# Kernel optimization log

Hardware: AMD Instinct MI355X
Metric: run time of the kernel (lower is better)

The kernel has to match this reference:

```python
import jax, jax.numpy as jnp
import numpy as np

EPS = 1e-5
SLOPE = 0.01  # torch LeakyReLU default

def _conv(x, w, b, stride):
    # x: [B,C,L], w: [O,I,3]
    y = jax.lax.conv_general_dilated(x, w, (stride,), [(1, 1)],
                                     dimension_numbers=("NCH", "OIH", "NCH"))
    return y + b[None, :, None]

def _bn(x, g, b, m, v):
    # eval-mode BatchNorm1d with running stats
    inv = jax.lax.rsqrt(v + EPS)
    return (x - m[None, :, None]) * (g * inv)[None, :, None] + b[None, :, None]

def _lrelu(x):
    return jnp.where(x >= 0, x, SLOPE * x)

def setup_inputs() -> dict:
    key = jax.random.key(0)
    ks = jax.random.split(key, 32)
    B, C, L = 32, 256, 2048
    K, D = 4096, 128
    d = {}
    d["x"] = jax.random.normal(ks[0], (B, C, L), dtype=jnp.float32)
    # conv weights [O,I,3]
    d["w1"] = jax.random.normal(ks[1], (256, 256, 3), jnp.float32) * 0.03
    d["b1"] = jax.random.normal(ks[2], (256,), jnp.float32) * 0.01
    d["w2"] = jax.random.normal(ks[3], (512, 256, 3), jnp.float32) * 0.03
    d["b2"] = jax.random.normal(ks[4], (512,), jnp.float32) * 0.01
    d["w3"] = jax.random.normal(ks[5], (512, 512, 3), jnp.float32) * 0.02
    d["b3"] = jax.random.normal(ks[6], (512,), jnp.float32) * 0.01
    d["w4"] = jax.random.normal(ks[7], (D, 512, 3), jnp.float32) * 0.02
    d["b4"] = jax.random.normal(ks[8], (D,), jnp.float32) * 0.01
    for i, ch in enumerate([256, 512, 512, D]):
        d[f"g{i+1}"] = 1.0 + 0.1 * jax.random.normal(ks[9 + 4 * i], (ch,), jnp.float32)
        d[f"be{i+1}"] = 0.1 * jax.random.normal(ks[10 + 4 * i], (ch,), jnp.float32)
        d[f"m{i+1}"] = 0.1 * jax.random.normal(ks[11 + 4 * i], (ch,), jnp.float32)
        d[f"v{i+1}"] = 0.5 + jax.random.uniform(ks[12 + 4 * i], (ch,), jnp.float32)
    d["emb"] = jax.random.uniform(ks[30], (K, D), jnp.float32,
                                  minval=-1.0 / K, maxval=1.0 / K)
    return d

def reference(x, w1, b1, w2, b2, w3, b3, w4, b4,
              g1, be1, m1, v1, g2, be2, m2, v2,
              g3, be3, m3, v3, g4, be4, m4, v4, emb):
    h = _lrelu(_bn(_conv(x, w1, b1, 2), g1, be1, m1, v1))   # [B,256,L/2]
    h = _lrelu(_bn(_conv(h, w2, b2, 2), g2, be2, m2, v2))   # [B,512,L/4]
    h = _lrelu(_bn(_conv(h, w3, b3, 2), g3, be3, m3, v3))   # [B,512,L/8]
    h = _lrelu(_bn(_conv(h, w4, b4, 1), g4, be4, m4, v4))   # [B,D,L/8]
    flat = jnp.transpose(h, (0, 2, 1)).reshape(-1, h.shape[1])  # [N,D]
    # squared-distance expansion: ||f||^2 + ||e||^2 - 2 f.e
    dist = (jnp.sum(flat * flat, axis=1, keepdims=True)
            + jnp.sum(emb * emb, axis=1)
            - 2.0 * flat @ emb.T)                            # [N,K]
    codes = jnp.argmin(dist, axis=1)
    return codes, dist
```

## Files before the change

kernel.cpp:

```cpp
#include <hip/hip_runtime.h>
#include <cstdint>
#include <math.h>

#define EPS_BN 1e-5f
#define SLOPE 0.01f
#define C14 6.103515625e-5f
#define SC14 16384.0f
#define HMIN 6.103515625e-5f

typedef __attribute__((ext_vector_type(8))) _Float16 half8;
typedef __attribute__((ext_vector_type(8))) short short8;
typedef __attribute__((ext_vector_type(16))) float f32x16;
typedef __attribute__((ext_vector_type(4))) float f32x4;

__device__ __forceinline__ void split16(float v, unsigned short& uh,
                                        unsigned short& ul) {
    _Float16 h = (_Float16)v;
    if (fabsf(v) < HMIN) h = (_Float16)0.0f;
    float rem = v - (float)h;
    _Float16 l = (_Float16)(rem * SC14);
    uh = __builtin_bit_cast(unsigned short, h);
    ul = __builtin_bit_cast(unsigned short, l);
}

typedef const __attribute__((address_space(1))) unsigned int* gas_ptr;
typedef __attribute__((address_space(3))) unsigned int* las_ptr;
__device__ __forceinline__ void glds16(const void* g, void* l) {
    __builtin_amdgcn_global_load_lds((gas_ptr)g, (las_ptr)l, 16, 0, 0);
}

template<int N>
__device__ __forceinline__ void vm_wait() {
    if constexpr (N == 0)      asm volatile("s_waitcnt vmcnt(0)" ::: "memory");
    else if constexpr (N == 8) asm volatile("s_waitcnt vmcnt(8)" ::: "memory");
    else if constexpr (N == 9) asm volatile("s_waitcnt vmcnt(9)" ::: "memory");
}
__device__ __forceinline__ void raw_bar() {
    asm volatile("" ::: "memory");
    __builtin_amdgcn_s_barrier();
    asm volatile("" ::: "memory");
}

__global__ __launch_bounds__(256)
void wprep_all(const float* __restrict__ w1, short* __restrict__ o1,
               const float* __restrict__ w2, short* __restrict__ o2,
               const float* __restrict__ w3, short* __restrict__ o3,
               const float* __restrict__ w4, short* __restrict__ o4)
{
    const float* w; short* wbuf; int CIN, COUT;
    switch (blockIdx.y) {
        case 0: w = w1; wbuf = o1; CIN = 256; COUT = 256; break;
        case 1: w = w2; wbuf = o2; CIN = 256; COUT = 512; break;
        case 2: w = w3; wbuf = o3; CIN = 512; COUT = 512; break;
        default: w = w4; wbuf = o4; CIN = 512; COUT = 128; break;
    }
    int KST = CIN / 16, OB = COUT / 128;
    int total = KST * OB * 1536;
    for (int sid = blockIdx.x * 256 + threadIdx.x; sid < total;
         sid += gridDim.x * 256) {
        int slot = sid % 1536;
        int kb = sid / 1536;
        int ob = kb % OB, ks = kb / OB;
        int m = slot & 31, hi = (slot >> 5) & 1, mf = (slot >> 6) & 3;
        int ts = slot >> 8;
        int t = ts >> 1, s = ts & 1;
        int oc = ob * 128 + mf * 32 + m;
        int ib = ks * 16 + hi * 8;
        short8 r;
        #pragma unroll
        for (int j = 0; j < 8; ++j) {
            float v = w[((size_t)oc * CIN + ib + j) * 3 + t];
            unsigned short uh, ul;
            split16(v, uh, ul);
            r[j] = (short)(s == 0 ? uh : ul);
        }
        *(short8*)(wbuf + (size_t)sid * 8) = r;
    }
}

__global__ __launch_bounds__(256)
void bnprep_init(
    const float* __restrict__ g1, const float* __restrict__ be1,
    const float* __restrict__ m1, const float* __restrict__ v1,
    const float* __restrict__ b1, float* __restrict__ sc1, float* __restrict__ off1,
    const float* __restrict__ g2, const float* __restrict__ be2,
    const float* __restrict__ m2, const float* __restrict__ v2,
    const float* __restrict__ b2, float* __restrict__ sc2, float* __restrict__ off2,
    const float* __restrict__ g3, const float* __restrict__ be3,
    const float* __restrict__ m3, const float* __restrict__ v3,
    const float* __restrict__ b3, float* __restrict__ sc3, float* __restrict__ off3,
    const float* __restrict__ g4, const float* __restrict__ be4,
    const float* __restrict__ m4, const float* __restrict__ v4,
    const float* __restrict__ b4, float* __restrict__ sc4, float* __restrict__ off4,
    unsigned long long* __restrict__ mp, float* __restrict__ sf)
{
    int bid = blockIdx.x;
    if (bid >= 38) { sf[(bid - 38) * 256 + threadIdx.x] = 0.0f; return; }
    if (bid >= 6) { mp[(bid - 6) * 256 + threadIdx.x] = ~0ULL; return; }
    const float *g, *be, *m, *v, *bias;
    float *sc, *off;
    int c;
    if (bid == 0) {
        g = g1; be = be1; m = m1; v = v1; bias = b1; sc = sc1; off = off1;
        c = threadIdx.x;
    } else if (bid <= 2) {
        g = g2; be = be2; m = m2; v = v2; bias = b2; sc = sc2; off = off2;
        c = (bid - 1) * 256 + threadIdx.x;
    } else if (bid <= 4) {
        g = g3; be = be3; m = m3; v = v3; bias = b3; sc = sc3; off = off3;
        c = (bid - 3) * 256 + threadIdx.x;
    } else {
        g = g4; be = be4; m = m4; v = v4; bias = b4; sc = sc4; off = off4;
        c = threadIdx.x;
        if (c >= 128) return;
    }
    float s = g[c] / sqrtf(v[c] + EPS_BN);
    sc[c] = s;
    off[c] = (bias[c] - m[c]) * s + be[c];
}

__global__ __launch_bounds__(256)
void xsplit(const float* __restrict__ x, short* __restrict__ xpl)
{
    const size_t PL = (size_t)32 * 32 * 2 * 1025 * 8;
    int l = blockIdx.x * 256 + threadIdx.x;
    int g = blockIdx.y, b = blockIdx.z;
    float v[8];
    #pragma unroll
    for (int j = 0; j < 8; ++j)
        v[j] = x[((size_t)b * 256 + g * 8 + j) * 2048 + l];
    int arr = l & 1;
    int slot = arr ? (l + 1) / 2 : l / 2 + 1;
    size_t base = ((((size_t)b * 32 + g) * 2 + arr) * 1025 + slot) * 8;
    short8 rh, rl;
    #pragma unroll
    for (int j = 0; j < 8; ++j) {
        unsigned short uh, ul;
        split16(v[j], uh, ul);
        rh[j] = (short)uh; rl[j] = (short)ul;
    }
    *(short8*)(xpl + base) = rh;
    *(short8*)(xpl + PL + base) = rl;
    if (l == 0) {
        short8 z;
        #pragma unroll
        for (int j = 0; j < 8; ++j) z[j] = 0;
        for (int sg = 0; sg < 2; ++sg)
            for (int a2 = 0; a2 < 2; ++a2)
                *(short8*)(xpl + sg * PL +
                           ((((size_t)b * 32 + g) * 2 + a2) * 1025) * 8) = z;
    }
}

template<int CIN, int COUT, int LIN, int TILE, int EPI>
__global__ __launch_bounds__(512, 1)
void conv_pair(const short* __restrict__ wbuf, const short* __restrict__ xpl,
               const float* __restrict__ scv, const float* __restrict__ offv,
               short* __restrict__ opl)
{
    constexpr int LOUT = LIN / 2;
    constexpr int KST = CIN / 16;
    constexpr int OBS = COUT / 128;
    constexpr int NG = CIN / 8;
    constexpr int SLOTS = LIN / 2 + 1;
    constexpr size_t PLIN = (size_t)32 * NG * 2 * SLOTS * 8;
    constexpr int NF = TILE / 64;
    constexpr int NGo = COUT / 8;
    constexpr int OSLOTS = (EPI == 0) ? (LOUT / 2 + 1) : (LOUT + 2);
    constexpr size_t PLOUT = (size_t)32 * NGo * ((EPI == 0) ? 2 : 1) * OSLOTS * 8;

    constexpr int XOFF = 49152;
    constexpr int BUF  = XOFF + 8 * 2112;
    constexpr int SCOFF = 2 * BUF;
    constexpr int SCNT = (TILE == 128) ? 9 : 8;
    __shared__ __align__(16) char lds[2 * BUF + 2048];

    const int tid = threadIdx.x;
    const int lane = tid & 63;
    const int wv = tid >> 6;
    const int wo = wv >> 2;
    const int wm = (wv >> 1) & 1, wn = wv & 1;
    const int hi = lane >> 5, n32 = lane & 31;
    const int n0 = blockIdx.x * TILE;
    const int oby = blockIdx.y;
    const int o0 = oby * 256;
    const int b = blockIdx.z;

    if (tid < 256) ((float*)(lds + SCOFF))[tid] = scv[o0 + tid];
    else ((float*)(lds + SCOFF + 1024))[tid - 256] = offv[o0 + tid - 256];

    f32x16 acc0[2][2], acc1[2][2];
    #pragma unroll
    for (int i = 0; i < 2; ++i)
        #pragma unroll
        for (int j = 0; j < 2; ++j)
            #pragma unroll
            for (int e = 0; e < 16; ++e) { acc0[i][j][e] = 0.0f; acc1[i][j][e] = 0.0f; }

    auto stage = [&](char* base, int ks) {
        const short* wsrc = wbuf + ((size_t)ks * OBS + (oby * 2 + wo)) * 1536 * 8;
        #pragma unroll
        for (int it = 0; it < 6; ++it) {
            int slot0 = it * 256 + (wv & 3) * 64;
            glds16(wsrc + (size_t)(slot0 + lane) * 8, base + wo * 24576 + slot0 * 16);
        }
        int g0 = ks * 2;
        int sg = wv >> 2, rhi = (wv >> 1) & 1, arr = wv & 1;
        int start = arr ? n0 : (n0 + 1);
        const short* src = xpl + (size_t)sg * PLIN
            + ((((size_t)b * NG + (g0 + rhi)) * 2 + arr) * SLOTS + start) * 8;
        char* dst = base + XOFF + ((sg * 2 + rhi) * 2 + arr) * 2112;
        if (TILE == 128) {
            glds16(src + (size_t)lane * 8, dst);
            glds16(src + (size_t)(64 + lane) * 8, dst + 64 * 16);
            int c2 = arr ? 65 : 64;
            glds16(src + (size_t)(c2 + lane) * 8, dst + c2 * 16);
        } else {
            glds16(src + (size_t)lane * 8, dst);
            int c1 = arr ? 1 : 0;
            glds16(src + (size_t)(c1 + lane) * 8, dst + c1 * 16);
        }
    };

    stage(lds, 0);

    #pragma unroll 1
    for (int ks = 0; ks < KST; ++ks) {
        char* cbase = lds + (ks & 1) * BUF;
        char* nbase = lds + ((ks & 1) ^ 1) * BUF;
        if (ks + 1 < KST) {
            stage(nbase, ks + 1);
            vm_wait<SCNT>();
        } else {
            vm_wait<0>();
        }
        raw_bar();
        __builtin_amdgcn_s_setprio(1);
        #pragma unroll
        for (int t = 0; t < 3; ++t) {
            half8 af[2][2], bx[2][2];
            #pragma unroll
            for (int s = 0; s < 2; ++s) {
                #pragma unroll
                for (int mf = 0; mf < 2; ++mf)
                    af[s][mf] = *(const half8*)(cbase + wo * 24576 +
                        (((t * 2 + s) * 4 + (wm * 2 + mf)) * 64 + lane) * 16);
                int arr = (t == 1) ? 0 : 1;
                int tof = (t == 2) ? 1 : 0;
                #pragma unroll
                for (int nf = 0; nf < NF; ++nf) {
                    int qb = wn * (TILE / 2) + nf * 32 + tof;
                    bx[s][nf] = *(const half8*)(cbase + XOFF + s * 8448
                                                + arr * 2112 + qb * 16
                                                + hi * 4224 + n32 * 16);
                }
            }
            #pragma unroll
            for (int mf = 0; mf < 2; ++mf)
                #pragma unroll
                for (int nf = 0; nf < NF; ++nf) {
                    acc0[mf][nf] = __builtin_amdgcn_mfma_f32_32x32x16_f16(
                        af[0][mf], bx[0][nf], acc0[mf][nf], 0, 0, 0);
                    acc1[mf][nf] = __builtin_amdgcn_mfma_f32_32x32x16_f16(
                        af[0][mf], bx[1][nf], acc1[mf][nf], 0, 0, 0);
                    acc1[mf][nf] = __builtin_amdgcn_mfma_f32_32x32x16_f16(
                        af[1][mf], bx[0][nf], acc1[mf][nf], 0, 0, 0);
                }
        }
        __builtin_amdgcn_s_setprio(0);
        raw_bar();
    }

    #pragma unroll
    for (int half = 0; half < NF; ++half) {
        __syncthreads();
        #pragma unroll
        for (int mf = 0; mf < 2; ++mf)
            #pragma unroll
            for (int r = 0; r < 16; ++r) {
                int ocl = mf * 32 + (r & 3) + 8 * (r >> 2) + 4 * hi;
                *(float*)(lds + wv * 8704 + n32 * 272 + ocl * 4) =
                    acc0[mf][half][r] + C14 * acc1[mf][half][r];
            }
        __syncthreads();
        #pragma unroll
        for (int it = 0; it < 4; ++it) {
            int sl = tid + it * 512;
            int w = sl >> 8, rem = sl & 255, p = rem >> 3, grp = rem & 7;
            int wo_ = w >> 2, wm_ = (w >> 1) & 1, wn_ = w & 1;
            f32x4 v0 = *(f32x4*)(lds + w * 8704 + p * 272 + grp * 32);
            f32x4 v1 = *(f32x4*)(lds + w * 8704 + p * 272 + grp * 32 + 16);
            int ocb = wo_ * 128 + wm_ * 64 + grp * 8;
            f32x4 s0 = *(f32x4*)(lds + SCOFF + ocb * 4);
            f32x4 s1 = *(f32x4*)(lds + SCOFF + ocb * 4 + 16);
            f32x4 q0 = *(f32x4*)(lds + SCOFF + 1024 + ocb * 4);
            f32x4 q1 = *(f32x4*)(lds + SCOFF + 1024 + ocb * 4 + 16);
            float y[8];
            #pragma unroll
            for (int j = 0; j < 4; ++j) {
                float a = v0[j] * s0[j] + q0[j];
                y[j] = a >= 0.0f ? a : SLOPE * a;
                float c = v1[j] * s1[j] + q1[j];
                y[4 + j] = c >= 0.0f ? c : SLOPE * c;
            }
            int pos_abs = n0 + wn_ * (TILE / 2) + half * 32 + p;
            int oc_abs = o0 + ocb;
            short8 rh, rl;
            #pragma unroll
            for (int j = 0; j < 8; ++j) {
                unsigned short uh, ul;
                split16(y[j], uh, ul);
                rh[j] = (short)uh; rl[j] = (short)ul;
            }
            int gq = oc_abs >> 3;
            size_t base;
            if (EPI == 0) {
                int arr = pos_abs & 1;
                int slot = arr ? (pos_abs + 1) / 2 : pos_abs / 2 + 1;
                base = ((((size_t)b * NGo + gq) * 2 + arr) * OSLOTS + slot) * 8;
            } else {
                base = (((size_t)b * NGo + gq) * OSLOTS + (pos_abs + 1)) * 8;
            }
            *(short8*)(opl + base) = rh;
            *(short8*)(opl + PLOUT + base) = rl;
        }
    }

    if (EPI == 0) {
        if (blockIdx.x == 0 && tid < 128) {
            int sg = tid >> 6, r2 = tid & 63, g16 = r2 >> 1, a2 = r2 & 1;
            int gq = oby * 32 + g16;
            short8 z;
            #pragma unroll
            for (int j = 0; j < 8; ++j) z[j] = 0;
            *(short8*)(opl + (size_t)sg * PLOUT +
                       ((((size_t)b * NGo + gq) * 2 + a2) * OSLOTS) * 8) = z;
        }
    } else {
        if (tid < 64 && (blockIdx.x == 0 || blockIdx.x == gridDim.x - 1)) {
            int sg = tid >> 5, g16 = tid & 31;
            int gq = oby * 32 + g16;
            int slot = (blockIdx.x == 0) ? 0 : (OSLOTS - 1);
            short8 z;
            #pragma unroll
            for (int j = 0; j < 8; ++j) z[j] = 0;
            *(short8*)(opl + (size_t)sg * PLOUT +
                       (((size_t)b * NGo + gq) * OSLOTS + slot) * 8) = z;
        }
    }
}

template<int CIN, int COUT, int LIN>
__global__ __launch_bounds__(256, 2)
void conv_s1(const short* __restrict__ wbuf, const short* __restrict__ xpl,
             const float* __restrict__ scv, const float* __restrict__ offv,
             short* __restrict__ fh, short* __restrict__ fl,
             float* __restrict__ sf)
{
    constexpr int KST = CIN / 16;
    constexpr int NG = CIN / 8;
    constexpr int SLOTS = LIN + 2;
    constexpr size_t PLIN = (size_t)32 * NG * SLOTS * 8;

    constexpr int XOFF = 24576;
    constexpr int BUF  = XOFF + 4 * 2112;
    constexpr int SCOFF = 2 * BUF;
    __shared__ __align__(16) char lds[2 * BUF + 1024];

    const int tid = threadIdx.x;
    const int lane = tid & 63;
    const int wv = tid >> 6;
    const int wm = wv >> 1, wn = wv & 1;
    const int hi = lane >> 5, n32 = lane & 31;
    const int n0 = blockIdx.x * 128;
    const int b = blockIdx.z;

    if (tid < 128) {
        ((float*)(lds + SCOFF))[tid] = scv[tid];
        ((float*)(lds + SCOFF + 512))[tid] = offv[tid];
    }

    f32x16 acc0[2][2], acc1[2][2];
    #pragma unroll
    for (int i = 0; i < 2; ++i)
        #pragma unroll
        for (int j = 0; j < 2; ++j)
            #pragma unroll
            for (int e = 0; e < 16; ++e) { acc0[i][j][e] = 0.0f; acc1[i][j][e] = 0.0f; }

    auto stage = [&](char* base, int ks) {
        const short* wsrc = wbuf + (size_t)ks * 1536 * 8;
        #pragma unroll
        for (int it = 0; it < 6; ++it) {
            int slot0 = it * 256 + wv * 64;
            glds16(wsrc + (size_t)(slot0 + lane) * 8, base + slot0 * 16);
        }
        int g0 = ks * 2;
        int sg = wv >> 1, rhi = wv & 1;
        const short* src = xpl + (size_t)sg * PLIN
            + (((size_t)b * NG + (g0 + rhi)) * SLOTS + n0) * 8;
        char* dst = base + XOFF + (sg * 2 + rhi) * 2112;
        glds16(src + (size_t)lane * 8, dst);
        glds16(src + (size_t)(64 + lane) * 8, dst + 64 * 16);
        glds16(src + (size_t)(66 + lane) * 8, dst + 66 * 16);
    };

    stage(lds, 0);

    #pragma unroll 1
    for (int ks = 0; ks < KST; ++ks) {
        char* cbase = lds + (ks & 1) * BUF;
        char* nbase = lds + ((ks & 1) ^ 1) * BUF;
        if (ks + 1 < KST) {
            stage(nbase, ks + 1);
            vm_wait<9>();
        } else {
            vm_wait<0>();
        }
        raw_bar();
        __builtin_amdgcn_s_setprio(1);
        #pragma unroll
        for (int t = 0; t < 3; ++t) {
            half8 af[2][2], bx[2][2];
            #pragma unroll
            for (int s = 0; s < 2; ++s) {
                #pragma unroll
                for (int mf = 0; mf < 2; ++mf)
                    af[s][mf] = *(const half8*)(cbase +
                        (((t * 2 + s) * 4 + (wm * 2 + mf)) * 64 + lane) * 16);
                #pragma unroll
                for (int nf = 0; nf < 2; ++nf) {
                    int qb = wn * 64 + nf * 32 + t;
                    bx[s][nf] = *(const half8*)(cbase + XOFF + s * 4224
                                                + qb * 16 + hi * 2112 + n32 * 16);
                }
            }
            #pragma unroll
            for (int mf = 0; mf < 2; ++mf)
                #pragma unroll
                for (int nf = 0; nf < 2; ++nf) {
                    acc0[mf][nf] = __builtin_amdgcn_mfma_f32_32x32x16_f16(
                        af[0][mf], bx[0][nf], acc0[mf][nf], 0, 0, 0);
                    acc1[mf][nf] = __builtin_amdgcn_mfma_f32_32x32x16_f16(
                        af[0][mf], bx[1][nf], acc1[mf][nf], 0, 0, 0);
                    acc1[mf][nf] = __builtin_amdgcn_mfma_f32_32x32x16_f16(
                        af[1][mf], bx[0][nf], acc1[mf][nf], 0, 0, 0);
                }
        }
        __builtin_amdgcn_s_setprio(0);
        raw_bar();
    }

    #pragma unroll
    for (int half = 0; half < 2; ++half) {
        __syncthreads();
        #pragma unroll
        for (int mf = 0; mf < 2; ++mf)
            #pragma unroll
            for (int r = 0; r < 16; ++r) {
                int ocl = mf * 32 + (r & 3) + 8 * (r >> 2) + 4 * hi;
                *(float*)(lds + wv * 8704 + n32 * 272 + ocl * 4) =
                    acc0[mf][half][r] + C14 * acc1[mf][half][r];
            }
        __syncthreads();
        #pragma unroll
        for (int it = 0; it < 4; ++it) {
            int sl = tid + it * 256;
            int w = sl >> 8, rem = sl & 255, p = rem >> 3, grp = rem & 7;
            int wm_ = w >> 1, wn_ = w & 1;
            f32x4 v0 = *(f32x4*)(lds + w * 8704 + p * 272 + grp * 32);
            f32x4 v1 = *(f32x4*)(lds + w * 8704 + p * 272 + grp * 32 + 16);
            int oclb = wm_ * 64 + grp * 8;
            f32x4 s0 = *(f32x4*)(lds + SCOFF + oclb * 4);
            f32x4 s1 = *(f32x4*)(lds + SCOFF + oclb * 4 + 16);
            f32x4 q0 = *(f32x4*)(lds + SCOFF + 512 + oclb * 4);
            f32x4 q1 = *(f32x4*)(lds + SCOFF + 512 + oclb * 4 + 16);
            float y[8];
            #pragma unroll
            for (int j = 0; j < 4; ++j) {
                float a = v0[j] * s0[j] + q0[j];
                y[j] = a >= 0.0f ? a : SLOPE * a;
                float c = v1[j] * s1[j] + q1[j];
                y[4 + j] = c >= 0.0f ? c : SLOPE * c;
            }
            int pos_abs = n0 + wn_ * 64 + half * 32 + p;
            int n = b * 256 + pos_abs;
            short8 rh, rl;
            float partial = 0.0f;
            #pragma unroll
            for (int j = 0; j < 8; ++j) {
                partial = fmaf(y[j], y[j], partial);
                unsigned short uh, ul;
                split16(y[j], uh, ul);
                rh[j] = (short)uh; rl[j] = (short)ul;
            }
            int g = wm_ * 8 + grp;
            size_t slot = ((((size_t)(n >> 5) * 8 + (g >> 1)) * 2 + (g & 1)) * 32
                           + (n & 31)) * 8;
            *(short8*)(fh + slot) = rh;
            *(short8*)(fl + slot) = rl;
            atomicAdd(sf + n, partial);
        }
    }
}

__global__ __launch_bounds__(256)
void split_kernel(const float* __restrict__ src, int nrows,
                  short* __restrict__ ph, short* __restrict__ pl,
                  float* __restrict__ sumv)
{
    int t = blockIdx.x * 256 + threadIdx.x;
    int n = t >> 4, g = t & 15;
    if (n >= nrows) return;
    const float* rowp = src + (size_t)n * 128 + g * 8;
    float4 v0 = *(const float4*)rowp;
    float4 v1 = *(const float4*)(rowp + 4);
    float vv[8] = {v0.x, v0.y, v0.z, v0.w, v1.x, v1.y, v1.z, v1.w};
    short8 rh, rl;
    float ss = 0.0f;
    #pragma unroll
    for (int j = 0; j < 8; ++j) {
        float v = vv[j];
        ss = fmaf(v, v, ss);
        unsigned short uh, ul;
        split16(v, uh, ul);
        rh[j] = (short)uh; rl[j] = (short)ul;
    }
    int nb = n >> 5, m = n & 31, ks = g >> 1, hi = g & 1;
    size_t slot = ((((size_t)nb * 8 + ks) * 2 + hi) * 32 + m) * 8;
    *(short8*)(ph + slot) = rh;
    *(short8*)(pl + slot) = rl;
    #pragma unroll
    for (int mk = 8; mk; mk >>= 1) ss += __shfl_xor(ss, mk);
    if (g == 0) sumv[n] = ss;
}

__global__ __launch_bounds__(256, 2)
void distmin_kernel(const short* __restrict__ fh, const short* __restrict__ fl,
                    const short* __restrict__ eh, const short* __restrict__ el,
                    const float* __restrict__ sf, const float* __restrict__ se,
                    float* __restrict__ dist, unsigned long long* __restrict__ mp)
{
    __shared__ unsigned long long cand[128 * 64];
    const int tid = threadIdx.x;
    const int lane = tid & 63;
    const int wv = tid >> 6;
    const int wm = wv >> 1, wn = wv & 1;
    const int hi = lane >> 5, n32 = lane & 31;
    const int kb = blockIdx.x;
    const int nb = blockIdx.y;

    f32x16 acc0[2][2], acc1[2][2];
    #pragma unroll
    for (int i = 0; i < 2; ++i)
        #pragma unroll
        for (int j = 0; j < 2; ++j)
            #pragma unroll
            for (int e = 0; e < 16; ++e) { acc0[i][j][e] = 0.0f; acc1[i][j][e] = 0.0f; }

    const short* fb[2][2];
    const short* eb[2][2];
    {
        const short* fpl[2] = {fh, fl};
        const short* epl[2] = {eh, el};
        #pragma unroll
        for (int s = 0; s < 2; ++s) {
            #pragma unroll
            for (int mf = 0; mf < 2; ++mf)
                fb[s][mf] = fpl[s] + (size_t)nb * 16384
                            + ((size_t)(wm * 2 + mf) * 8 * 64 + lane) * 8;
            #pragma unroll
            for (int nf = 0; nf < 2; ++nf)
                eb[s][nf] = epl[s]
                            + ((size_t)(kb * 4 + wn * 2 + nf) * 8 * 64 + lane) * 8;
        }
    }

    #pragma unroll
    for (int ks = 0; ks < 8; ++ks) {
        half8 af[2][2], bx[2][2];
        #pragma unroll
        for (int s = 0; s < 2; ++s) {
            #pragma unroll
            for (int mf = 0; mf < 2; ++mf)
                af[s][mf] = *(const half8*)(fb[s][mf] + ks * 512);
            #pragma unroll
            for (int nf = 0; nf < 2; ++nf)
                bx[s][nf] = *(const half8*)(eb[s][nf] + ks * 512);
        }
        #pragma unroll
        for (int mf = 0; mf < 2; ++mf)
            #pragma unroll
            for (int nf = 0; nf < 2; ++nf) {
                acc0[mf][nf] = __builtin_amdgcn_mfma_f32_32x32x16_f16(
                    af[0][mf], bx[0][nf], acc0[mf][nf], 0, 0, 0);
                acc1[mf][nf] = __builtin_amdgcn_mfma_f32_32x32x16_f16(
                    af[0][mf], bx[1][nf], acc1[mf][nf], 0, 0, 0);
                acc1[mf][nf] = __builtin_amdgcn_mfma_f32_32x32x16_f16(
                    af[1][mf], bx[0][nf], acc1[mf][nf], 0, 0, 0);
            }
    }

    const int n_blk = nb * 128;
    const int kc0 = kb * 128 + wn * 64 + n32;
    const float se0 = se[kc0];
    const float se1 = se[kc0 + 32];
    #pragma unroll
    for (int mf = 0; mf < 2; ++mf) {
        #pragma unroll
        for (int r = 0; r < 16; ++r) {
            int nloc = wm * 64 + mf * 32 + (r & 3) + 8 * (r >> 2) + 4 * hi;
            int n = n_blk + nloc;
            float sfn = sf[n];
            float d0 = acc0[mf][0][r] + C14 * acc1[mf][0][r];
            float d1 = acc0[mf][1][r] + C14 * acc1[mf][1][r];
            float v0 = (sfn + se0) - 2.0f * d0;
            float v1 = (sfn + se1) - 2.0f * d1;
            __builtin_nontemporal_store(v0, &dist[(size_t)n * 4096 + kc0]);
            __builtin_nontemporal_store(v1, &dist[(size_t)n * 4096 + kc0 + 32]);
            unsigned long long p0 =
                (((unsigned long long)__float_as_uint(v0)) << 32) | (unsigned)kc0;
            unsigned long long p1 =
                (((unsigned long long)__float_as_uint(v1)) << 32) | (unsigned)(kc0 + 32);
            unsigned long long p = p1 < p0 ? p1 : p0;
            cand[nloc * 64 + wn * 32 + n32] = p;
        }
    }
    __syncthreads();
    {
        int row = tid >> 1, h = tid & 1;
        unsigned long long best = ~0ULL;
        #pragma unroll
        for (int i = 0; i < 32; ++i) {
            int c = h * 32 + ((i + row) & 31);
            unsigned long long cv = cand[row * 64 + c];
            best = cv < best ? cv : best;
        }
        unsigned lo = (unsigned)best, hw = (unsigned)(best >> 32);
        unsigned lo2 = __shfl_xor(lo, 1), hw2 = __shfl_xor(hw, 1);
        unsigned long long ob = (((unsigned long long)hw2) << 32) | lo2;
        if (ob < best) best = ob;
        if (h == 0) atomicMin(mp + n_blk + row, best);
    }
}

__global__ __launch_bounds__(256)
void codes_kernel(const unsigned long long* __restrict__ mp,
                  float* __restrict__ codes)
{
    int n = blockIdx.x * 256 + threadIdx.x;
    if (n < 8192) codes[n] = (float)(unsigned)(mp[n] & 0xffffffffULL);
}

extern "C" void kernel_launch(void* const* d_in, const int* in_sizes, int n_in,
                              void* d_out, int out_size, void* d_ws, size_t ws_size,
                              hipStream_t stream)
{
    const float* x   = (const float*)d_in[0];
    const float* w1  = (const float*)d_in[1];
    const float* b1  = (const float*)d_in[2];
    const float* w2  = (const float*)d_in[3];
    const float* b2  = (const float*)d_in[4];
    const float* w3  = (const float*)d_in[5];
    const float* b3  = (const float*)d_in[6];
    const float* w4  = (const float*)d_in[7];
    const float* b4  = (const float*)d_in[8];
    const float* g1  = (const float*)d_in[9];
    const float* be1 = (const float*)d_in[10];
    const float* m1  = (const float*)d_in[11];
    const float* v1  = (const float*)d_in[12];
    const float* g2  = (const float*)d_in[13];
    const float* be2 = (const float*)d_in[14];
    const float* m2  = (const float*)d_in[15];
    const float* v2  = (const float*)d_in[16];
    const float* g3  = (const float*)d_in[17];
    const float* be3 = (const float*)d_in[18];
    const float* m3  = (const float*)d_in[19];
    const float* v3  = (const float*)d_in[20];
    const float* g4  = (const float*)d_in[21];
    const float* be4 = (const float*)d_in[22];
    const float* m4  = (const float*)d_in[23];
    const float* v4  = (const float*)d_in[24];
    const float* emb = (const float*)d_in[25];

    float* outf  = (float*)d_out;
    float* codes = outf;
    float* distm = outf + 8192;

    char* wsb = (char*)d_ws;
    short* wb1 = (short*)(wsb + 0);
    short* wb2 = (short*)(wsb + 786432);
    short* wb3 = (short*)(wsb + 2359296);
    short* wb4 = (short*)(wsb + 5505024);
    float* sc1 = (float*)(wsb + 6291456); float* off1 = sc1 + 256;
    float* sc2 = (float*)(wsb + 6293504); float* off2 = sc2 + 512;
    float* sc3 = (float*)(wsb + 6297600); float* off3 = sc3 + 512;
    float* sc4 = (float*)(wsb + 6301696); float* off4 = sc4 + 128;
    short* h1p = (short*)(wsb + 6302720);
    short* fh  = (short*)(wsb + 39922688);
    short* fl  = (short*)(wsb + 42019840);
    short* eh  = (short*)(wsb + 44116992);
    short* el  = (short*)(wsb + 45165568);
    float* sf  = (float*)(wsb + 46214144);
    float* se  = (float*)(wsb + 46246912);
    unsigned long long* mp = (unsigned long long*)(wsb + 46263296);

    char* db = (char*)distm;
    short* xpl = (short*)db;
    short* h2p = (short*)db;
    short* h3p = (short*)(db + 33685504);

    wprep_all<<<dim3(192, 4), 256, 0, stream>>>(w1, wb1, w2, wb2, w3, wb3, w4, wb4);
    bnprep_init<<<70, 256, 0, stream>>>(
        g1, be1, m1, v1, b1, sc1, off1,
        g2, be2, m2, v2, b2, sc2, off2,
        g3, be3, m3, v3, b3, sc3, off3,
        g4, be4, m4, v4, b4, sc4, off4, mp, sf);
    split_kernel<<<256, 256, 0, stream>>>(emb, 4096, eh, el, se);

    xsplit<<<dim3(8, 32, 32), 256, 0, stream>>>(x, xpl);
    conv_pair<256, 256, 2048, 128, 0>
        <<<dim3(8, 1, 32), 512, 0, stream>>>(wb1, xpl, sc1, off1, h1p);
    conv_pair<256, 512, 1024, 128, 0>
        <<<dim3(4, 2, 32), 512, 0, stream>>>(wb2, h1p, sc2, off2, h2p);
    conv_pair<512, 512, 512, 64, 1>
        <<<dim3(4, 2, 32), 512, 0, stream>>>(wb3, h2p, sc3, off3, h3p);
    conv_s1<512, 128, 256>
        <<<dim3(2, 1, 32), 256, 0, stream>>>(wb4, h3p, sc4, off4, fh, fl, sf);

    distmin_kernel<<<dim3(32, 64), 256, 0, stream>>>(fh, fl, eh, el,
                                                     sf, se, distm, mp);
    codes_kernel<<<32, 256, 0, stream>>>(mp, codes);
}
```

Baseline: 261.4 us.

## Fuse input split into first conv, use register-staged prefetch, halve conv4 tile

The standalone xsplit kernel is removed. The first conv now reads raw fp32 input, splits it into fp16 high/low parts and writes them to LDS itself, which avoids a full write and re-read of the split input in global memory. All conv kernels switch from direct global-to-LDS loads to a register-staged scheme: the next stage is loaded into registers during the MFMA work and written to LDS afterwards, followed by __syncthreads. The final stride-1 conv uses 64-wide tiles, doubling its grid from 64 to 128 blocks. The register staging raises register pressure and drops the async LDS-load path, which could hurt the heavier conv kernels.

```diff
diff --git a/kernel.cpp b/kernel.cpp
--- a/kernel.cpp
+++ b/kernel.cpp
@@ -21,24 +21,6 @@
     _Float16 l = (_Float16)(rem * SC14);
     uh = __builtin_bit_cast(unsigned short, h);
     ul = __builtin_bit_cast(unsigned short, l);
-}
-
-typedef const __attribute__((address_space(1))) unsigned int* gas_ptr;
-typedef __attribute__((address_space(3))) unsigned int* las_ptr;
-__device__ __forceinline__ void glds16(const void* g, void* l) {
-    __builtin_amdgcn_global_load_lds((gas_ptr)g, (las_ptr)l, 16, 0, 0);
-}
-
-template<int N>
-__device__ __forceinline__ void vm_wait() {
-    if constexpr (N == 0)      asm volatile("s_waitcnt vmcnt(0)" ::: "memory");
-    else if constexpr (N == 8) asm volatile("s_waitcnt vmcnt(8)" ::: "memory");
-    else if constexpr (N == 9) asm volatile("s_waitcnt vmcnt(9)" ::: "memory");
-}
-__device__ __forceinline__ void raw_bar() {
-    asm volatile("" ::: "memory");
-    __builtin_amdgcn_s_barrier();
-    asm volatile("" ::: "memory");
 }
 
 __global__ __launch_bounds__(256)
@@ -119,42 +101,10 @@
     off[c] = (bias[c] - m[c]) * s + be[c];
 }
 
-__global__ __launch_bounds__(256)
-void xsplit(const float* __restrict__ x, short* __restrict__ xpl)
-{
-    const size_t PL = (size_t)32 * 32 * 2 * 1025 * 8;
-    int l = blockIdx.x * 256 + threadIdx.x;
-    int g = blockIdx.y, b = blockIdx.z;
-    float v[8];
-    #pragma unroll
-    for (int j = 0; j < 8; ++j)
-        v[j] = x[((size_t)b * 256 + g * 8 + j) * 2048 + l];
-    int arr = l & 1;
-    int slot = arr ? (l + 1) / 2 : l / 2 + 1;
-    size_t base = ((((size_t)b * 32 + g) * 2 + arr) * 1025 + slot) * 8;
-    short8 rh, rl;
-    #pragma unroll
-    for (int j = 0; j < 8; ++j) {
-        unsigned short uh, ul;
-        split16(v[j], uh, ul);
-        rh[j] = (short)uh; rl[j] = (short)ul;
-    }
-    *(short8*)(xpl + base) = rh;
-    *(short8*)(xpl + PL + base) = rl;
-    if (l == 0) {
-        short8 z;
-        #pragma unroll
-        for (int j = 0; j < 8; ++j) z[j] = 0;
-        for (int sg = 0; sg < 2; ++sg)
-            for (int a2 = 0; a2 < 2; ++a2)
-                *(short8*)(xpl + sg * PL +
-                           ((((size_t)b * 32 + g) * 2 + a2) * 1025) * 8) = z;
-    }
-}
-
-template<int CIN, int COUT, int LIN, int TILE, int EPI>
+template<int CIN, int COUT, int LIN, int TILE, int EPI, int SRC>
 __global__ __launch_bounds__(512, 1)
 void conv_pair(const short* __restrict__ wbuf, const short* __restrict__ xpl,
+               const float* __restrict__ xraw,
                const float* __restrict__ scv, const float* __restrict__ offv,
                short* __restrict__ opl)
 {
@@ -172,7 +122,6 @@
     constexpr int XOFF = 49152;
     constexpr int BUF  = XOFF + 8 * 2112;
     constexpr int SCOFF = 2 * BUF;
-    constexpr int SCNT = (TILE == 128) ? 9 : 8;
     __shared__ __align__(16) char lds[2 * BUF + 2048];
 
     const int tid = threadIdx.x;
@@ -197,44 +146,98 @@
             #pragma unroll
             for (int e = 0; e < 16; ++e) { acc0[i][j][e] = 0.0f; acc1[i][j][e] = 0.0f; }
 
-    auto stage = [&](char* base, int ks) {
+    short8 rw[6];
+    short8 rxa, rxb, rxc;
+    float rf[8], rf2[8];
+
+    auto stage_load = [&](int ks) {
         const short* wsrc = wbuf + ((size_t)ks * OBS + (oby * 2 + wo)) * 1536 * 8;
         #pragma unroll
-        for (int it = 0; it < 6; ++it) {
-            int slot0 = it * 256 + (wv & 3) * 64;
-            glds16(wsrc + (size_t)(slot0 + lane) * 8, base + wo * 24576 + slot0 * 16);
-        }
-        int g0 = ks * 2;
-        int sg = wv >> 2, rhi = (wv >> 1) & 1, arr = wv & 1;
-        int start = arr ? n0 : (n0 + 1);
-        const short* src = xpl + (size_t)sg * PLIN
-            + ((((size_t)b * NG + (g0 + rhi)) * 2 + arr) * SLOTS + start) * 8;
-        char* dst = base + XOFF + ((sg * 2 + rhi) * 2 + arr) * 2112;
-        if (TILE == 128) {
-            glds16(src + (size_t)lane * 8, dst);
-            glds16(src + (size_t)(64 + lane) * 8, dst + 64 * 16);
-            int c2 = arr ? 65 : 64;
-            glds16(src + (size_t)(c2 + lane) * 8, dst + c2 * 16);
+        for (int it = 0; it < 6; ++it)
+            rw[it] = *(const short8*)(wsrc +
+                      (size_t)(it * 256 + (wv & 3) * 64 + lane) * 8);
+        if constexpr (SRC == 0) {
+            int sg = wv >> 2, rhi = (wv >> 1) & 1, arr = wv & 1;
+            int start = arr ? n0 : (n0 + 1);
+            const short* src = xpl + (size_t)sg * PLIN
+                + ((((size_t)b * NG + (ks * 2 + rhi)) * 2 + arr) * SLOTS + start) * 8;
+            rxa = *(const short8*)(src + (size_t)lane * 8);
+            if constexpr (TILE == 128) {
+                rxb = *(const short8*)(src + (size_t)(64 + lane) * 8);
+                if (arr && lane == 0)
+                    rxc = *(const short8*)(src + (size_t)128 * 8);
+            } else {
+                if (arr && lane == 0)
+                    rxb = *(const short8*)(src + (size_t)64 * 8);
+            }
         } else {
-            glds16(src + (size_t)lane * 8, dst);
-            int c1 = arr ? 1 : 0;
-            glds16(src + (size_t)(c1 + lane) * 8, dst + c1 * 16);
+            int run = wv & 3, rhi = run >> 1, arr = run & 1, hs = wv >> 2;
+            int c = hs * 64 + lane;
+            int l = arr ? (2 * (n0 + c) - 1) : (2 * (n0 + c));
+            const float* xr = xraw + ((size_t)(b * 256 + ks * 16 + rhi * 8)) * 2048;
+            #pragma unroll
+            for (int j = 0; j < 8; ++j)
+                rf[j] = (l >= 0) ? xr[(size_t)j * 2048 + l] : 0.0f;
+            if (arr && hs == 1 && lane == 0) {
+                int l2 = 2 * (n0 + 128) - 1;
+                #pragma unroll
+                for (int j = 0; j < 8; ++j)
+                    rf2[j] = xr[(size_t)j * 2048 + l2];
+            }
         }
     };
 
-    stage(lds, 0);
+    auto stage_write = [&](char* base) {
+        #pragma unroll
+        for (int it = 0; it < 6; ++it)
+            *(short8*)(base + wo * 24576 +
+                       (it * 256 + (wv & 3) * 64 + lane) * 16) = rw[it];
+        if constexpr (SRC == 0) {
+            int sg = wv >> 2, rhi = (wv >> 1) & 1, arr = wv & 1;
+            char* dst = base + XOFF + ((sg * 2 + rhi) * 2 + arr) * 2112;
+            *(short8*)(dst + lane * 16) = rxa;
+            if constexpr (TILE == 128) {
+                *(short8*)(dst + (64 + lane) * 16) = rxb;
+                if (arr && lane == 0) *(short8*)(dst + 128 * 16) = rxc;
+            } else {
+                if (arr && lane == 0) *(short8*)(dst + 64 * 16) = rxb;
+            }
+        } else {
+            int run = wv & 3, rhi = run >> 1, arr = run & 1, hs = wv >> 2;
+            int c = hs * 64 + lane;
+            short8 rh, rl;
+            #pragma unroll
+            for (int j = 0; j < 8; ++j) {
+                unsigned short uh, ul;
+                split16(rf[j], uh, ul);
+                rh[j] = (short)uh; rl[j] = (short)ul;
+            }
+            char* dst = base + XOFF + (rhi * 2 + arr) * 2112;
+            *(short8*)(dst + c * 16) = rh;
+            *(short8*)(dst + 8448 + c * 16) = rl;
+            if (arr && hs == 1 && lane == 0) {
+                short8 rh2, rl2;
+                #pragma unroll
+                for (int j = 0; j < 8; ++j) {
+                    unsigned short uh, ul;
+                    split16(rf2[j], uh, ul);
+                    rh2[j] = (short)uh; rl2[j] = (short)ul;
+                }
+                *(short8*)(dst + 128 * 16) = rh2;
+                *(short8*)(dst + 8448 + 128 * 16) = rl2;
+            }
+        }
+    };
+
+    stage_load(0);
+    stage_write(lds);
+    __syncthreads();
 
     #pragma unroll 1
     for (int ks = 0; ks < KST; ++ks) {
-        char* cbase = lds + (ks & 1) * BUF;
-        char* nbase = lds + ((ks & 1) ^ 1) * BUF;
-        if (ks + 1 < KST) {
-            stage(nbase, ks + 1);
-            vm_wait<SCNT>();
-        } else {
-            vm_wait<0>();
-        }
-        raw_bar();
+        const char* cbase = lds + (ks & 1) * BUF;
+        bool more = (ks + 1 < KST);
+        if (more) stage_load(ks + 1);
         __builtin_amdgcn_s_setprio(1);
         #pragma unroll
         for (int t = 0; t < 3; ++t) {
@@ -268,7 +271,8 @@
                 }
         }
         __builtin_amdgcn_s_setprio(0);
-        raw_bar();
+        if (more) stage_write(lds + ((ks + 1) & 1) * BUF);
+        __syncthreads();
     }
 
     #pragma unroll
@@ -361,6 +365,7 @@
     constexpr int NG = CIN / 8;
     constexpr int SLOTS = LIN + 2;
     constexpr size_t PLIN = (size_t)32 * NG * SLOTS * 8;
+    constexpr int TILE = 64;
 
     constexpr int XOFF = 24576;
     constexpr int BUF  = XOFF + 4 * 2112;
@@ -372,7 +377,7 @@
     const int wv = tid >> 6;
     const int wm = wv >> 1, wn = wv & 1;
     const int hi = lane >> 5, n32 = lane & 31;
-    const int n0 = blockIdx.x * 128;
+    const int n0 = blockIdx.x * TILE;
     const int b = blockIdx.z;
 
     if (tid < 128) {
@@ -380,127 +385,121 @@
         ((float*)(lds + SCOFF + 512))[tid] = offv[tid];
     }
 
-    f32x16 acc0[2][2], acc1[2][2];
+    f32x16 acc0[2], acc1[2];
     #pragma unroll
     for (int i = 0; i < 2; ++i)
         #pragma unroll
-        for (int j = 0; j < 2; ++j)
-            #pragma unroll
-            for (int e = 0; e < 16; ++e) { acc0[i][j][e] = 0.0f; acc1[i][j][e] = 0.0f; }
-
-    auto stage = [&](char* base, int ks) {
+        for (int e = 0; e < 16; ++e) { acc0[i][e] = 0.0f; acc1[i][e] = 0.0f; }
+
+    short8 rw[6], rxa, rxb;
+
+    auto stage_load = [&](int ks) {
         const short* wsrc = wbuf + (size_t)ks * 1536 * 8;
         #pragma unroll
-        for (int it = 0; it < 6; ++it) {
-            int slot0 = it * 256 + wv * 64;
-            glds16(wsrc + (size_t)(slot0 + lane) * 8, base + slot0 * 16);
-        }
-        int g0 = ks * 2;
+        for (int it = 0; it < 6; ++it)
+            rw[it] = *(const short8*)(wsrc +
+                      (size_t)(it * 256 + wv * 64 + lane) * 8);
         int sg = wv >> 1, rhi = wv & 1;
         const short* src = xpl + (size_t)sg * PLIN
-            + (((size_t)b * NG + (g0 + rhi)) * SLOTS + n0) * 8;
+            + (((size_t)b * NG + (ks * 2 + rhi)) * SLOTS + n0) * 8;
+        rxa = *(const short8*)(src + (size_t)lane * 8);
+        if (lane < 2) rxb = *(const short8*)(src + (size_t)(64 + lane) * 8);
+    };
+    auto stage_write = [&](char* base) {
+        #pragma unroll
+        for (int it = 0; it < 6; ++it)
+            *(short8*)(base + (it * 256 + wv * 64 + lane) * 16) = rw[it];
+        int sg = wv >> 1, rhi = wv & 1;
         char* dst = base + XOFF + (sg * 2 + rhi) * 2112;
-        glds16(src + (size_t)lane * 8, dst);
-        glds16(src + (size_t)(64 + lane) * 8, dst + 64 * 16);
-        glds16(src + (size_t)(66 + lane) * 8, dst + 66 * 16);
+        *(short8*)(dst + lane * 16) = rxa;
+        if (lane < 2) *(short8*)(dst + (64 + lane) * 16) = rxb;
     };
 
-    stage(lds, 0);
+    stage_load(0);
+    stage_write(lds);
+    __syncthreads();
 
     #pragma unroll 1
     for (int ks = 0; ks < KST; ++ks) {
-        char* cbase = lds + (ks & 1) * BUF;
-        char* nbase = lds + ((ks & 1) ^ 1) * BUF;
-        if (ks + 1 < KST) {
-            stage(nbase, ks + 1);
-            vm_wait<9>();
-        } else {
-            vm_wait<0>();
-        }
-        raw_bar();
+        const char* cbase = lds + (ks & 1) * BUF;
+        bool more = (ks + 1 < KST);
+        if (more) stage_load(ks + 1);
         __builtin_amdgcn_s_setprio(1);
         #pragma unroll
         for (int t = 0; t < 3; ++t) {
-            half8 af[2][2], bx[2][2];
+            half8 af[2][2], bx[2];
             #pragma unroll
             for (int s = 0; s < 2; ++s) {
                 #pragma unroll
                 for (int mf = 0; mf < 2; ++mf)
                     af[s][mf] = *(const half8*)(cbase +
                         (((t * 2 + s) * 4 + (wm * 2 + mf)) * 64 + lane) * 16);
-                #pragma unroll
-                for (int nf = 0; nf < 2; ++nf) {
-                    int qb = wn * 64 + nf * 32 + t;
-                    bx[s][nf] = *(const half8*)(cbase + XOFF + s * 4224
-                                                + qb * 16 + hi * 2112 + n32 * 16);
-                }
-            }
-            #pragma unroll
-            for (int mf = 0; mf < 2; ++mf)
-                #pragma unroll
-                for (int nf = 0; nf < 2; ++nf) {
-                    acc0[mf][nf] = __builtin_amdgcn_mfma_f32_32x32x16_f16(
-                        af[0][mf], bx[0][nf], acc0[mf][nf], 0, 0, 0);
-                    acc1[mf][nf] = __builtin_amdgcn_mfma_f32_32x32x16_f16(
-                        af[0][mf], bx[1][nf], acc1[mf][nf], 0, 0, 0);
-                    acc1[mf][nf] = __builtin_amdgcn_mfma_f32_32x32x16_f16(
-                        af[1][mf], bx[0][nf], acc1[mf][nf], 0, 0, 0);
-                }
+                int qb = wn * 32 + t;
+                bx[s] = *(const half8*)(cbase + XOFF + s * 4224
+                                        + qb * 16 + hi * 2112 + n32 * 16);
+            }
+            #pragma unroll
+            for (int mf = 0; mf < 2; ++mf) {
+                acc0[mf] = __builtin_amdgcn_mfma_f32_32x32x16_f16(
+                    af[0][mf], bx[0], acc0[mf], 0, 0, 0);
+                acc1[mf] = __builtin_amdgcn_mfma_f32_32x32x16_f16(
+                    af[0][mf], bx[1], acc1[mf], 0, 0, 0);
+                acc1[mf] = __builtin_amdgcn_mfma_f32_32x32x16_f16(
+                    af[1][mf], bx[0], acc1[mf], 0, 0, 0);
+            }
         }
         __builtin_amdgcn_s_setprio(0);
-        raw_bar();
-    }
-
-    #pragma unroll
-    for (int half = 0; half < 2; ++half) {
+        if (more) stage_write(lds + ((ks + 1) & 1) * BUF);
         __syncthreads();
-        #pragma unroll
-        for (int mf = 0; mf < 2; ++mf)
-            #pragma unroll
-            for (int r = 0; r < 16; ++r) {
-                int ocl = mf * 32 + (r & 3) + 8 * (r >> 2) + 4 * hi;
-                *(float*)(lds + wv * 8704 + n32 * 272 + ocl * 4) =
-                    acc0[mf][half][r] + C14 * acc1[mf][half][r];
-            }
-        __syncthreads();
-        #pragma unroll
-        for (int it = 0; it < 4; ++it) {
-            int sl = tid + it * 256;
-            int w = sl >> 8, rem = sl & 255, p = rem >> 3, grp = rem & 7;
-            int wm_ = w >> 1, wn_ = w & 1;
-            f32x4 v0 = *(f32x4*)(lds + w * 8704 + p * 272 + grp * 32);
-            f32x4 v1 = *(f32x4*)(lds + w * 8704 + p * 272 + grp * 32 + 16);
-            int oclb = wm_ * 64 + grp * 8;
-            f32x4 s0 = *(f32x4*)(lds + SCOFF + oclb * 4);
-            f32x4 s1 = *(f32x4*)(lds + SCOFF + oclb * 4 + 16);
-            f32x4 q0 = *(f32x4*)(lds + SCOFF + 512 + oclb * 4);
-            f32x4 q1 = *(f32x4*)(lds + SCOFF + 512 + oclb * 4 + 16);
-            float y[8];
-            #pragma unroll
-            for (int j = 0; j < 4; ++j) {
-                float a = v0[j] * s0[j] + q0[j];
-                y[j] = a >= 0.0f ? a : SLOPE * a;
-                float c = v1[j] * s1[j] + q1[j];
-                y[4 + j] = c >= 0.0f ? c : SLOPE * c;
-            }
-            int pos_abs = n0 + wn_ * 64 + half * 32 + p;
-            int n = b * 256 + pos_abs;
-            short8 rh, rl;
-            float partial = 0.0f;
-            #pragma unroll
-            for (int j = 0; j < 8; ++j) {
-                partial = fmaf(y[j], y[j], partial);
-                unsigned short uh, ul;
-                split16(y[j], uh, ul);
-                rh[j] = (short)uh; rl[j] = (short)ul;
-            }
-            int g = wm_ * 8 + grp;
-            size_t slot = ((((size_t)(n >> 5) * 8 + (g >> 1)) * 2 + (g & 1)) * 32
-                           + (n & 31)) * 8;
-            *(short8*)(fh + slot) = rh;
-            *(short8*)(fl + slot) = rl;
-            atomicAdd(sf + n, partial);
-        }
+    }
+
+    __syncthreads();
+    #pragma unroll
+    for (int mf = 0; mf < 2; ++mf)
+        #pragma unroll
+        for (int r = 0; r < 16; ++r) {
+            int ocl = mf * 32 + (r & 3) + 8 * (r >> 2) + 4 * hi;
+            *(float*)(lds + wv * 8704 + n32 * 272 + ocl * 4) =
+                acc0[mf][r] + C14 * acc1[mf][r];
+        }
+    __syncthreads();
+    #pragma unroll
+    for (int it = 0; it < 4; ++it) {
+        int sl = tid + it * 256;
+        int w = sl >> 8, rem = sl & 255, p = rem >> 3, grp = rem & 7;
+        int wm_ = w >> 1, wn_ = w & 1;
+        f32x4 v0 = *(f32x4*)(lds + w * 8704 + p * 272 + grp * 32);
+        f32x4 v1 = *(f32x4*)(lds + w * 8704 + p * 272 + grp * 32 + 16);
+        int oclb = wm_ * 64 + grp * 8;
+        f32x4 s0 = *(f32x4*)(lds + SCOFF + oclb * 4);
+        f32x4 s1 = *(f32x4*)(lds + SCOFF + oclb * 4 + 16);
+        f32x4 q0 = *(f32x4*)(lds + SCOFF + 512 + oclb * 4);
+        f32x4 q1 = *(f32x4*)(lds + SCOFF + 512 + oclb * 4 + 16);
+        float y[8];
+        #pragma unroll
+        for (int j = 0; j < 4; ++j) {
+            float a = v0[j] * s0[j] + q0[j];
+            y[j] = a >= 0.0f ? a : SLOPE * a;
+            float c = v1[j] * s1[j] + q1[j];
+            y[4 + j] = c >= 0.0f ? c : SLOPE * c;
+        }
+        int pos_abs = n0 + wn_ * 32 + p;
+        int n = b * 256 + pos_abs;
+        short8 rh, rl;
+        float partial = 0.0f;
+        #pragma unroll
+        for (int j = 0; j < 8; ++j) {
+            partial = fmaf(y[j], y[j], partial);
+            unsigned short uh, ul;
+            split16(y[j], uh, ul);
+            rh[j] = (short)uh; rl[j] = (short)ul;
+        }
+        int g = wm_ * 8 + grp;
+        size_t slot = ((((size_t)(n >> 5) * 8 + (g >> 1)) * 2 + (g & 1)) * 32
+                       + (n & 31)) * 8;
+        *(short8*)(fh + slot) = rh;
+        *(short8*)(fl + slot) = rl;
+        atomicAdd(sf + n, partial);
     }
 }
 
@@ -706,7 +705,6 @@
     unsigned long long* mp = (unsigned long long*)(wsb + 46263296);
 
     char* db = (char*)distm;
-    short* xpl = (short*)db;
     short* h2p = (short*)db;
     short* h3p = (short*)(db + 33685504);
 
@@ -718,15 +716,14 @@
         g4, be4, m4, v4, b4, sc4, off4, mp, sf);
     split_kernel<<<256, 256, 0, stream>>>(emb, 4096, eh, el, se);
 
-    xsplit<<<dim3(8, 32, 32), 256, 0, stream>>>(x, xpl);
-    conv_pair<256, 256, 2048, 128, 0>
-        <<<dim3(8, 1, 32), 512, 0, stream>>>(wb1, xpl, sc1, off1, h1p);
-    conv_pair<256, 512, 1024, 128, 0>
-        <<<dim3(4, 2, 32), 512, 0, stream>>>(wb2, h1p, sc2, off2, h2p);
-    conv_pair<512, 512, 512, 64, 1>
-        <<<dim3(4, 2, 32), 512, 0, stream>>>(wb3, h2p, sc3, off3, h3p);
+    conv_pair<256, 256, 2048, 128, 0, 1>
+        <<<dim3(8, 1, 32), 512, 0, stream>>>(wb1, nullptr, x, sc1, off1, h1p);
+    conv_pair<256, 512, 1024, 128, 0, 0>
+        <<<dim3(4, 2, 32), 512, 0, stream>>>(wb2, h1p, nullptr, sc2, off2, h2p);
+    conv_pair<512, 512, 512, 64, 1, 0>
+        <<<dim3(4, 2, 32), 512, 0, stream>>>(wb3, h2p, nullptr, sc3, off3, h3p);
     conv_s1<512, 128, 256>
-        <<<dim3(2, 1, 32), 256, 0, stream>>>(wb4, h3p, sc4, off4, fh, fl, sf);
+        <<<dim3(4, 1, 32), 256, 0, stream>>>(wb4, h3p, sc4, off4, fh, fl, sf);
 
     distmin_kernel<<<dim3(32, 64), 256, 0, stream>>>(fh, fl, eh, el,
                                                      sf, se, distm, mp);
```

Result: faster. 235.1 us (-10.1%).
